# Optimization experiments

Hardware: AMD Instinct MI355X
Metric: run time of the kernel (lower is better)

## Reference

```python
import jax, jax.numpy as jnp
import numpy as np

H = 16          # num_attention_heads
DH = 64         # attention_head_size = hidden // heads
WINDOW = 128    # window_size
GLOBAL_RATIO = 0.1
SCALE = 1.0 / np.sqrt(DH)


def _combined_mask(seq_len):
    # sliding window: |i-j| <= window_size // 2
    pos = jnp.arange(seq_len)
    dist = pos[None, :] - pos[:, None]
    window_mask = jnp.abs(dist) <= (WINDOW // 2)
    # global tokens: first max(1, int(S * ratio)) positions, full row+col
    num_global = max(1, int(seq_len * GLOBAL_RATIO))
    is_global = pos < num_global
    global_mask = is_global[:, None] | is_global[None, :]
    return window_mask | global_mask  # [S, S] bool


def setup_inputs() -> dict:
    key = jax.random.key(0)
    ks = jax.random.split(key, 9)
    B, S, Dm = 2, 2048, 1024
    s = 0.02
    return {
        "hidden_states": jax.random.normal(ks[0], (B, S, Dm), jnp.float32),
        "Wq": jax.random.normal(ks[1], (Dm, Dm), jnp.float32) * s,
        "bq": jax.random.normal(ks[2], (Dm,), jnp.float32) * s,
        "Wk": jax.random.normal(ks[3], (Dm, Dm), jnp.float32) * s,
        "bk": jax.random.normal(ks[4], (Dm,), jnp.float32) * s,
        "Wv": jax.random.normal(ks[5], (Dm, Dm), jnp.float32) * s,
        "bv": jax.random.normal(ks[6], (Dm,), jnp.float32) * s,
        "Wo": jax.random.normal(ks[7], (Dm, Dm), jnp.float32) * s,
        "bo": jax.random.normal(ks[8], (Dm,), jnp.float32) * s,
    }


def reference(hidden_states, Wq, bq, Wk, bk, Wv, bv, Wo, bo):
    B, S, Dm = hidden_states.shape

    def heads(x):  # [B,S,Dm] -> [B,H,S,Dh]
        return x.reshape(B, S, H, DH).transpose(0, 2, 1, 3)

    q = heads(hidden_states @ Wq.T + bq)
    k = heads(hidden_states @ Wk.T + bk)
    v = heads(hidden_states @ Wv.T + bv)

    scores = jnp.einsum("bhqd,bhkd->bhqk", q, k) * SCALE
    mask = _combined_mask(S)  # [S,S] bool, True = attend
    scores = scores + jnp.where(mask, 0.0, -10000.0)[None, None]

    probs = jax.nn.softmax(scores, axis=-1)
    ctx = jnp.einsum("bhqk,bhkd->bhqd", probs, v)
    ctx = ctx.transpose(0, 2, 1, 3).reshape(B, S, Dm)
    return ctx @ Wo.T + bo
```

## Files before the change

### kernel.cpp

```cpp
#include <hip/hip_runtime.h>


#define B_   2
#define S_   2048
#define DM   1024
#define H_   16
#define NG   204
#define BS_  4096
#define SCL2 0.1803368801111204f
#define NEGF -3.0e38f

typedef unsigned short u16;
typedef unsigned int   u32;
typedef __attribute__((ext_vector_type(8))) short frag8;
typedef __attribute__((ext_vector_type(4))) short frag4;
typedef __attribute__((ext_vector_type(4))) float f32x4;

#define MFMA16(A, Bf, C) __builtin_amdgcn_mfma_f32_16x16x32_bf16((A), (Bf), (C), 0, 0, 0)

__device__ __forceinline__ f32x4 mfma_16x16x16_bf16(frag4 a, frag4 b, f32x4 c) {
#if defined(__HIP_DEVICE_COMPILE__)
  return __builtin_amdgcn_mfma_f32_16x16x16bf16_1k(a, b, c, 0, 0, 0);
#else
  (void)a; (void)b;
  return c;
#endif
}

#define GLD16(g, l)                                                              \
  __builtin_amdgcn_global_load_lds((const __attribute__((address_space(1))) u32*)(g), \
                                   (__attribute__((address_space(3))) u32*)(l), 16, 0, 0)
#define EXP2(x) exp2f(x)

__device__ __forceinline__ u16 f2bf(float f) {
  union { float f; u32 u; } c; c.f = f;
  u32 u = c.u + 0x7fffu + ((c.u >> 16) & 1u);
  return (u16)(u >> 16);
}

#if defined(__HIP_DEVICE_COMPILE__)
__device__ __forceinline__ u32 cvtpk_bf16(float lo, float hi) {
  u32 r;
  asm("v_cvt_pk_bf16_f32 %0, %1, %2" : "=v"(r) : "v"(lo), "v"(hi));
  return r;
}
#else
__device__ __forceinline__ u32 cvtpk_bf16(float lo, float hi) { (void)lo; (void)hi; return 0; }
#endif

__device__ __forceinline__ frag4 pack4_bf16(float a, float b, float c, float d) {
  union { u32 u[2]; frag4 f; } x;
  x.u[0] = cvtpk_bf16(a, b);
  x.u[1] = cvtpk_bf16(c, d);
  return x.f;
}

__global__ void cvt_all(const float* __restrict__ X,  const float* __restrict__ Wq,
                        const float* __restrict__ Wk, const float* __restrict__ Wv,
                        const float* __restrict__ Wo,
                        u16* Xb, u16* Wqb, u16* Wkb, u16* Wvb, u16* Wob) {
  const int chunk = blockIdx.y;
  const float* src; u16* dst;
  if (chunk < 4)      { src = X + (size_t)chunk * 1048576; dst = Xb + (size_t)chunk * 1048576; }
  else if (chunk == 4){ src = Wq; dst = Wqb; }
  else if (chunk == 5){ src = Wk; dst = Wkb; }
  else if (chunk == 6){ src = Wv; dst = Wvb; }
  else                { src = Wo; dst = Wob; }
  int i = blockIdx.x * 256 + threadIdx.x;
  float4 v = ((const float4*)src)[i];
  u32 lo = (u32)f2bf(v.x) | ((u32)f2bf(v.y) << 16);
  u32 hi = (u32)f2bf(v.z) | ((u32)f2bf(v.w) << 16);
  ((uint2*)dst)[i] = make_uint2(lo, hi);
}

__device__ __forceinline__ void gemm_mainloop(const u16* __restrict__ A, const u16* __restrict__ Bm,
                                              int bm, int bn, u16* As, u16* Bs,
                                              f32x4 acc[4][4]) {
  const int tid = threadIdx.x;
  const int wv = tid >> 6, lane = tid & 63, l15 = lane & 15, quad = lane >> 4;
  const int wm = wv & 1, wn = wv >> 1;

  const u16* gA[4]; const u16* gB[4];
#pragma unroll
  for (int c = 0; c < 4; ++c) {
    int idx = (wv * 4 + c) * 64 + lane;
    int r = idx >> 3;
    int cb = (idx & 7) ^ (r & 7);
    gA[c] = A  + (size_t)(bm + r) * DM + cb * 8;
    gB[c] = Bm + (size_t)(bn + r) * DM + cb * 8;
  }

  int offA[4][2], offB[4][2];
#pragma unroll
  for (int i = 0; i < 4; ++i)
#pragma unroll
    for (int h = 0; h < 2; ++h) {
      int mA = wm * 64 + i * 16 + l15;
      int mB = wn * 64 + i * 16 + l15;
      int cb = (quad + h * 4) ^ (l15 & 7);
      offA[i][h] = ((mA << 3) + cb) << 4;
      offB[i][h] = ((mB << 3) + cb) << 4;
    }

  for (int k0 = 0; k0 < DM; k0 += 64) {
#pragma unroll
    for (int c = 0; c < 4; ++c) {
      GLD16(gA[c] + k0, (char*)As + (wv * 4 + c) * 1024);
      GLD16(gB[c] + k0, (char*)Bs + (wv * 4 + c) * 1024);
    }
    __syncthreads();
    frag8 af[4][2], bf[4][2];
#pragma unroll
    for (int i = 0; i < 4; ++i) {
      af[i][0] = *(const frag8*)((const char*)As + offA[i][0]);
      af[i][1] = *(const frag8*)((const char*)As + offA[i][1]);
      bf[i][0] = *(const frag8*)((const char*)Bs + offB[i][0]);
      bf[i][1] = *(const frag8*)((const char*)Bs + offB[i][1]);
    }
#pragma unroll
    for (int h = 0; h < 2; ++h)
#pragma unroll
      for (int i = 0; i < 4; ++i)
#pragma unroll
        for (int j = 0; j < 4; ++j)
          acc[i][j] = MFMA16(af[i][h], bf[j][h], acc[i][j]);
    __syncthreads();
  }
}

__global__ __launch_bounds__(256, 3) void gemm_qkv(const u16* __restrict__ Xb,
    const u16* __restrict__ Wqb, const u16* __restrict__ Wkb, const u16* __restrict__ Wvb,
    const float* __restrict__ bq, const float* __restrict__ bk, const float* __restrict__ bv,
    u16* __restrict__ Qb, u16* __restrict__ Kb, u16* __restrict__ Vt) {
  __shared__ u16 As[8192], Bs[8192];
  const int bm = blockIdx.y * 128;
  const int which = blockIdx.x >> 3;
  const int bnl = (blockIdx.x & 7) * 128;
  const u16* W = (which == 0) ? Wqb : (which == 1) ? Wkb : Wvb;
  const float* bias = (which == 0) ? bq : (which == 1) ? bk : bv;

  f32x4 acc[4][4] = {};
  gemm_mainloop(Xb, W, bm, bnl, As, Bs, acc);

  const int tid = threadIdx.x, wv = tid >> 6, lane = tid & 63, l15 = lane & 15, quad = lane >> 4;
  const int wm = wv & 1, wn = wv >> 1;
  if (which < 2) {
    u16* O = (which == 0) ? Qb : Kb;
    const float scl = (which == 0) ? SCL2 : 1.0f;
#pragma unroll
    for (int j = 0; j < 4; ++j) {
      int col = bnl + wn * 64 + j * 16 + l15;
      float bb = bias[col];
#pragma unroll
      for (int i = 0; i < 4; ++i) {
        int row0 = bm + wm * 64 + i * 16 + quad * 4;
#pragma unroll
        for (int r = 0; r < 4; ++r)
          O[(size_t)(row0 + r) * DM + col] = f2bf((acc[i][j][r] + bb) * scl);
      }
    }
  } else {
#pragma unroll
    for (int j = 0; j < 4; ++j) {
      int col = bnl + wn * 64 + j * 16 + l15;
      float bb = bias[col];
#pragma unroll
      for (int i = 0; i < 4; ++i) {
        int row0 = bm + wm * 64 + i * 16 + quad * 4;
        u32 lo = (u32)f2bf(acc[i][j][0] + bb) | ((u32)f2bf(acc[i][j][1] + bb) << 16);
        u32 hi = (u32)f2bf(acc[i][j][2] + bb) | ((u32)f2bf(acc[i][j][3] + bb) << 16);
        *(uint2*)&Vt[(size_t)col * BS_ + row0] = make_uint2(lo, hi);
      }
    }
  }
}

__global__ __launch_bounds__(256, 3) void gemm_wo(const u16* __restrict__ Cx,
    const u16* __restrict__ Wob, const float* __restrict__ bo, float* __restrict__ out) {
  __shared__ u16 As[4096], Bs[8192];
  const int tid = threadIdx.x;
  const int wv = tid >> 6, lane = tid & 63, l15 = lane & 15, quad = lane >> 4;
  const int bm = blockIdx.y * 64, bn = blockIdx.x * 128;

  const u16* gA[2]; const u16* gB[4];
  int ldsA[2], ldsB[4];
#pragma unroll
  for (int c = 0; c < 2; ++c) {
    int slot = c * 256 + wv * 64 + lane;
    int r = slot >> 3, cb = (slot & 7) ^ (r & 7);
    gA[c] = Cx + (size_t)(bm + r) * DM + cb * 8;
    ldsA[c] = (c * 256 + wv * 64) * 16;
  }
#pragma unroll
  for (int c = 0; c < 4; ++c) {
    int slot = c * 256 + wv * 64 + lane;
    int r = slot >> 3, cb = (slot & 7) ^ (r & 7);
    gB[c] = Wob + (size_t)(bn + r) * DM + cb * 8;
    ldsB[c] = (c * 256 + wv * 64) * 16;
  }

  int offA[2], offB[8][2];
#pragma unroll
  for (int h = 0; h < 2; ++h) {
    int rowA = wv * 16 + l15;
    offA[h] = ((rowA << 3) + ((quad + h * 4) ^ (l15 & 7))) << 4;
#pragma unroll
    for (int j = 0; j < 8; ++j) {
      int rowB = j * 16 + l15;
      offB[j][h] = ((rowB << 3) + ((quad + h * 4) ^ (l15 & 7))) << 4;
    }
  }

  f32x4 acc[8] = {};
  for (int k0 = 0; k0 < DM; k0 += 64) {
#pragma unroll
    for (int c = 0; c < 2; ++c) GLD16(gA[c] + k0, (char*)As + ldsA[c]);
#pragma unroll
    for (int c = 0; c < 4; ++c) GLD16(gB[c] + k0, (char*)Bs + ldsB[c]);
    __syncthreads();
    frag8 af0 = *(const frag8*)((const char*)As + offA[0]);
    frag8 af1 = *(const frag8*)((const char*)As + offA[1]);
#pragma unroll
    for (int j = 0; j < 8; ++j) {
      frag8 bf0 = *(const frag8*)((const char*)Bs + offB[j][0]);
      frag8 bf1 = *(const frag8*)((const char*)Bs + offB[j][1]);
      acc[j] = MFMA16(af0, bf0, acc[j]);
      acc[j] = MFMA16(af1, bf1, acc[j]);
    }
    __syncthreads();
  }

#pragma unroll
  for (int j = 0; j < 8; ++j) {
    int col = bn + j * 16 + l15;
    float bb = bo[col];
    int row0 = bm + wv * 16 + quad * 4;
#pragma unroll
    for (int r = 0; r < 4; ++r)
      out[(size_t)(row0 + r) * DM + col] = acc[j][r] + bb;
  }
}

__global__ __launch_bounds__(256, 3) void attn_kernel(const u16* __restrict__ Q,
                                                      const u16* __restrict__ K,
                                                      const u16* __restrict__ Vt,
                                                      u16* __restrict__ Ctx,
                                                      float* __restrict__ Op,
                                                      float* __restrict__ Lp) {
  __shared__ u16 Ks[2][4096];
  __shared__ u16 Vs[2][4096];

  const int tid = threadIdx.x, w = tid >> 6, lane = tid & 63, l15 = lane & 15, quad = lane >> 4;
  const int blk = blockIdx.x;
  const int bh = blk & 31, unit = blk >> 5;
  const int b = bh >> 4, h = bh & 15;
  const bool heavy = unit < 8;
  const int strip = heavy ? (unit >> 2) : 0;
  const int q0 = heavy ? strip * 128 : 256 + (unit - 8) * 128;
  const int qw = q0 + w * 16;

  frag8 bq[2][2];
#pragma unroll
  for (int g = 0; g < 2; ++g) {
    const u16* qrow = Q + (size_t)(b * S_ + qw + g * 64 + l15) * DM + h * 64;
    bq[g][0] = *(const frag8*)(qrow + quad * 8);
    bq[g][1] = *(const frag8*)(qrow + quad * 8 + 32);
  }

  const u16* gK[2]; const u16* gV[2]; int ldso[2];
#pragma unroll
  for (int c = 0; c < 2; ++c) {
    int sl = (w * 2 + c) * 64 + lane;
    int r = sl >> 3;
    int fr = (r & 7) ^ (((r >> 3) & 1) << 2);
    int cb = (sl & 7) ^ fr;
    gK[c] = K  + (size_t)(b * S_ + r) * DM + h * 64 + cb * 8;
    gV[c] = Vt + (size_t)(h * 64 + r) * BS_ + (size_t)b * S_ + cb * 8;
    ldso[c] = (w * 2 + c) * 1024;
  }

  const int fl = (l15 & 7) ^ (((l15 >> 3) & 1) << 2);
  int offKb[2];
#pragma unroll
  for (int hh = 0; hh < 2; ++hh)
    offKb[hh] = ((l15 << 3) + ((quad + hh * 4) ^ fl)) << 4;
  int offVb[4];
#pragma unroll
  for (int kg = 0; kg < 4; ++kg)
    offVb[kg] = ((((l15 << 3) + ((((kg << 1) | (quad >> 1))) ^ fl)) << 4)
                 | ((quad & 1) << 3));

  int mlo[2]; u32 mspan[2];
#pragma unroll
  for (int g = 0; g < 2; ++g) {
    int qi = qw + g * 64 + l15;
    bool qg = qi < NG;
    mlo[g]   = qg ? (int)0x80000000 : (qi - 64);
    mspan[g] = qg ? 0xFFFFFFFFu : 128u;
  }
  const frag4 ones = {(short)0x3F80, (short)0x3F80, (short)0x3F80, (short)0x3F80};

  f32x4 o[2][4] = {};
  f32x4 o_l[2] = {};

  auto stage = [&](int t, int buf) {
#pragma unroll
    for (int c = 0; c < 2; ++c) {
      GLD16(gK[c] + (size_t)t * 64 * DM, (char*)Ks[buf] + ldso[c]);
      GLD16(gV[c] + t * 64,              (char*)Vs[buf] + ldso[c]);
    }
  };

  auto step = [&](int kt, int p, int mmode) {
    int gok0 = 1, gok1 = 1;
    if (mmode == 1) {
      const int k0s = kt * 64;
      const int ql1 = qw + 64;
      gok0 = (qw  < NG) || ((k0s + 63 >= qw  - 64) && (k0s <= qw  + 79));
      gok1 = (ql1 < NG) || ((k0s + 63 >= ql1 - 64) && (k0s <= ql1 + 79));
      if (!(gok0 | gok1)) return;
    }
    const char* kb_ = (const char*)Ks[p];
    const char* vb_ = (const char*)Vs[p];
    frag8 ak[4][2];
#pragma unroll
    for (int kg = 0; kg < 4; ++kg) {
      ak[kg][0] = *(const frag8*)(kb_ + offKb[0] + kg * 2048);
      ak[kg][1] = *(const frag8*)(kb_ + offKb[1] + kg * 2048);
    }
    const int k0 = kt * 64;
    const int gok[2] = {gok0, gok1};
    frag4 pk[2][4];
#pragma unroll
    for (int g = 0; g < 2; ++g) {
      if (!gok[g]) continue;
      f32x4 st[4] = {};
#pragma unroll
      for (int kg = 0; kg < 4; ++kg) {
        st[kg] = MFMA16(ak[kg][0], bq[g][0], st[kg]);
        st[kg] = MFMA16(ak[kg][1], bq[g][1], st[kg]);
      }
      if (mmode) {
#pragma unroll
        for (int kg = 0; kg < 4; ++kg) {
          float pr[4];
#pragma unroll
          for (int r = 0; r < 4; ++r) {
            int kc = k0 + kg * 16 + quad * 4 + r;
            bool act = ((u32)(kc - mlo[g]) <= mspan[g]);
            if (mmode == 2) act = act || (kc < NG);
            float e = EXP2(st[kg][r]);
            pr[r] = act ? e : 0.0f;
          }
          pk[g][kg] = pack4_bf16(pr[0], pr[1], pr[2], pr[3]);
        }
      } else {
#pragma unroll
        for (int kg = 0; kg < 4; ++kg)
          pk[g][kg] = pack4_bf16(EXP2(st[kg][0]), EXP2(st[kg][1]),
                                 EXP2(st[kg][2]), EXP2(st[kg][3]));
      }
    }
    if (gok0 & gok1) {
#pragma unroll
      for (int kg = 0; kg < 4; ++kg) {
        o_l[0] = mfma_16x16x16_bf16(ones, pk[0][kg], o_l[0]);
        o_l[1] = mfma_16x16x16_bf16(ones, pk[1][kg], o_l[1]);
#pragma unroll
        for (int nt = 0; nt < 4; ++nt) {
          frag4 av = *(const frag4*)(vb_ + offVb[kg] + nt * 2048);
          o[0][nt] = mfma_16x16x16_bf16(av, pk[0][kg], o[0][nt]);
          o[1][nt] = mfma_16x16x16_bf16(av, pk[1][kg], o[1][nt]);
        }
      }
    } else if (gok0) {
#pragma unroll
      for (int kg = 0; kg < 4; ++kg) {
        o_l[0] = mfma_16x16x16_bf16(ones, pk[0][kg], o_l[0]);
#pragma unroll
        for (int nt = 0; nt < 4; ++nt) {
          frag4 av = *(const frag4*)(vb_ + offVb[kg] + nt * 2048);
          o[0][nt] = mfma_16x16x16_bf16(av, pk[0][kg], o[0][nt]);
        }
      }
    } else {
#pragma unroll
      for (int kg = 0; kg < 4; ++kg) {
        o_l[1] = mfma_16x16x16_bf16(ones, pk[1][kg], o_l[1]);
#pragma unroll
        for (int nt = 0; nt < 4; ++nt) {
          frag4 av = *(const frag4*)(vb_ + offVb[kg] + nt * 2048);
          o[1][nt] = mfma_16x16x16_bf16(av, pk[1][kg], o[1][nt]);
        }
      }
    }
  };

  if (heavy) {
    const int seg = unit & 3;
    const int kt0 = seg * 8;
    const bool dm = (strip == 1);
    int p = 0;
    stage(kt0, 0);
#pragma unroll 1
    for (int tt = 0; tt < 8; ++tt) {
      __syncthreads();
      if (tt < 7) stage(kt0 + tt + 1, p ^ 1);
      const int kt = kt0 + tt;
      const int mm = dm ? ((kt == 3) ? 2 : ((kt > 2) ? 1 : 0)) : 0;
      step(kt, p, mm);
      p ^= 1;
    }
    float* op = Op + ((size_t)((bh * 2 + strip) * 4 + seg)) * 8192;
    float* lp = Lp + ((size_t)((bh * 2 + strip) * 4 + seg)) * 128;
#pragma unroll
    for (int g = 0; g < 2; ++g) {
      int rl = g * 64 + w * 16 + l15;
      if (quad == 0) lp[rl] = o_l[g][0];
#pragma unroll
      for (int nt = 0; nt < 4; ++nt)
        *(float4*)&op[rl * 64 + nt * 16 + quad * 4] =
            make_float4(o[g][nt][0], o[g][nt][1], o[g][nt][2], o[g][nt][3]);
    }
    return;
  }

  auto activef = [&](int t) {
    int k0 = t * 64;
    return (k0 < NG) || (k0 + 63 >= q0 - 64 && k0 <= q0 + 127 + 64);
  };
  auto nextt = [&](int cur) { int n = cur + 1; while (n < 32 && !activef(n)) ++n; return n; };

  int kt = 0, p = 0;
  stage(0, 0);
  for (;;) {
    int ktn = nextt(kt);
    bool more = ktn < 32;
    __syncthreads();
    if (more) stage(ktn, p ^ 1);
    const int mm = (kt == 3) ? 2 : ((kt > 2) ? 1 : 0);
    step(kt, p, mm);
    if (!more) break;
    kt = ktn; p ^= 1;
  }

#pragma unroll
  for (int g = 0; g < 2; ++g) {
    float inv = 1.0f / o_l[g][0];
    u16* crow = Ctx + (size_t)((size_t)b * S_ + qw + g * 64 + l15) * DM + h * 64;
#pragma unroll
    for (int nt = 0; nt < 4; ++nt) {
      u32 lo = (u32)f2bf(o[g][nt][0] * inv) | ((u32)f2bf(o[g][nt][1] * inv) << 16);
      u32 hi = (u32)f2bf(o[g][nt][2] * inv) | ((u32)f2bf(o[g][nt][3] * inv) << 16);
      *(uint2*)&crow[nt * 16 + quad * 4] = make_uint2(lo, hi);
    }
  }
}

__global__ __launch_bounds__(256) void combine_kernel(const float* __restrict__ Op,
                                                      const float* __restrict__ Lp,
                                                      u16* __restrict__ Ctx) {
  const int blk = blockIdx.x;
  const int bh = blk & 31, s64 = blk >> 5;
  const int b = bh >> 4, h = bh & 15;
  const int t = threadIdx.x;
  const int row = t >> 2, colg = (t & 3) * 16;
  const int gq = s64 * 64 + row;
  const int strip = gq >> 7, rIn = gq & 127;

  const float* opb = Op + ((size_t)(bh * 2 + strip) * 4) * 8192;
  const float* lpb = Lp + ((size_t)(bh * 2 + strip) * 4) * 128;

  float l = lpb[rIn] + lpb[128 + rIn] + lpb[256 + rIn] + lpb[384 + rIn];
  float acc[16];
#pragma unroll
  for (int e = 0; e < 16; ++e) acc[e] = opb[rIn * 64 + colg + e];
#pragma unroll
  for (int seg = 1; seg < 4; ++seg)
#pragma unroll
    for (int e = 0; e < 16; ++e) acc[e] += opb[seg * 8192 + rIn * 64 + colg + e];

  float inv = 1.0f / l;
  u32 pk[8];
#pragma unroll
  for (int p = 0; p < 8; ++p)
    pk[p] = (u32)f2bf(acc[2 * p] * inv) | ((u32)f2bf(acc[2 * p + 1] * inv) << 16);
  u16* dst = Ctx + (size_t)((size_t)b * S_ + gq) * DM + h * 64 + colg;
  *(uint4*)dst       = make_uint4(pk[0], pk[1], pk[2], pk[3]);
  *(uint4*)(dst + 8) = make_uint4(pk[4], pk[5], pk[6], pk[7]);
}

extern "C" void kernel_launch(void* const* d_in, const int* in_sizes, int n_in,
                              void* d_out, int out_size, void* d_ws, size_t ws_size,
                              hipStream_t stream) {
  const float* X  = (const float*)d_in[0];
  const float* Wq = (const float*)d_in[1];
  const float* bq = (const float*)d_in[2];
  const float* Wk = (const float*)d_in[3];
  const float* bk = (const float*)d_in[4];
  const float* Wv = (const float*)d_in[5];
  const float* bv = (const float*)d_in[6];
  const float* Wo = (const float*)d_in[7];
  const float* bo = (const float*)d_in[8];
  float* out = (float*)d_out;

  u16* ws = (u16*)d_ws;
  const size_t NX = (size_t)BS_ * DM;
  const size_t NW = (size_t)DM * DM;
  u16* Xb  = ws;
  u16* Wqb = Xb + NX;
  u16* Wkb = Wqb + NW;
  u16* Wvb = Wkb + NW;
  u16* Wob = Wvb + NW;
  u16* Qb  = Wob + NW;
  u16* Kb  = Qb + NX;
  u16* Vt  = Kb + NX;
  u16* Cx  = Vt + NX;
  float* Op = (float*)(Cx + NX);
  float* Lp = Op + (size_t)32 * 2 * 4 * 8192;

  cvt_all<<<dim3(1024, 8), 256, 0, stream>>>(X, Wq, Wk, Wv, Wo, Xb, Wqb, Wkb, Wvb, Wob);
  gemm_qkv<<<dim3(24, 32), 256, 0, stream>>>(Xb, Wqb, Wkb, Wvb, bq, bk, bv, Qb, Kb, Vt);
  attn_kernel<<<22 * 32, 256, 0, stream>>>(Qb, Kb, Vt, Cx, Op, Lp);
  combine_kernel<<<128, 256, 0, stream>>>(Op, Lp, Cx);
  gemm_wo<<<dim3(8, 64), 256, 0, stream>>>(Cx, Wob, bo, out);
}
```

Baseline: 173.9 us.

## Rewrite QKV projection GEMM with 256x192 tiles and double-buffered interleaved pipeline

Replaces the 128x128 single-buffered QKV GEMM with a 512-thread, 256x192-tile kernel. It treats the contiguous Wq/Wk/Wv bf16 buffers as one fused 3072-row weight matrix. Global-to-LDS loads are double-buffered with prefetch two steps ahead and interleaved between MFMA phases, using explicit barriers, waitcnts and setprio. A swizzled workgroup ID is added for L2 locality. The aim is to hide load latency and raise arithmetic intensity, at the cost of more LDS and registers, and it relies on the weight buffers being adjacent.

```diff
diff --git a/kernel.cpp b/kernel.cpp
--- a/kernel.cpp
+++ b/kernel.cpp
@@ -53,6 +53,16 @@
   x.u[0] = cvtpk_bf16(a, b);
   x.u[1] = cvtpk_bf16(c, d);
   return x.f;
+}
+
+__device__ __forceinline__ void wait_lgkm0() {
+  asm volatile("s_waitcnt lgkmcnt(0)" ::: "memory");
+  __builtin_amdgcn_sched_barrier(0);
+}
+__device__ __forceinline__ void hbar() {
+  __builtin_amdgcn_sched_barrier(0);
+  __builtin_amdgcn_s_barrier();
+  __builtin_amdgcn_sched_barrier(0);
 }
 
 __global__ void cvt_all(const float* __restrict__ X,  const float* __restrict__ Wq,
@@ -73,103 +83,184 @@
   ((uint2*)dst)[i] = make_uint2(lo, hi);
 }
 
-__device__ __forceinline__ void gemm_mainloop(const u16* __restrict__ A, const u16* __restrict__ Bm,
-                                              int bm, int bn, u16* As, u16* Bs,
-                                              f32x4 acc[4][4]) {
-  const int tid = threadIdx.x;
-  const int wv = tid >> 6, lane = tid & 63, l15 = lane & 15, quad = lane >> 4;
-  const int wm = wv & 1, wn = wv >> 1;
-
-  const u16* gA[4]; const u16* gB[4];
-#pragma unroll
-  for (int c = 0; c < 4; ++c) {
-    int idx = (wv * 4 + c) * 64 + lane;
-    int r = idx >> 3;
-    int cb = (idx & 7) ^ (r & 7);
-    gA[c] = A  + (size_t)(bm + r) * DM + cb * 8;
-    gB[c] = Bm + (size_t)(bn + r) * DM + cb * 8;
-  }
-
-  int offA[4][2], offB[4][2];
-#pragma unroll
-  for (int i = 0; i < 4; ++i)
-#pragma unroll
-    for (int h = 0; h < 2; ++h) {
-      int mA = wm * 64 + i * 16 + l15;
-      int mB = wn * 64 + i * 16 + l15;
-      int cb = (quad + h * 4) ^ (l15 & 7);
-      offA[i][h] = ((mA << 3) + cb) << 4;
-      offB[i][h] = ((mB << 3) + cb) << 4;
-    }
-
-  for (int k0 = 0; k0 < DM; k0 += 64) {
-#pragma unroll
-    for (int c = 0; c < 4; ++c) {
-      GLD16(gA[c] + k0, (char*)As + (wv * 4 + c) * 1024);
-      GLD16(gB[c] + k0, (char*)Bs + (wv * 4 + c) * 1024);
-    }
-    __syncthreads();
-    frag8 af[4][2], bf[4][2];
-#pragma unroll
-    for (int i = 0; i < 4; ++i) {
-      af[i][0] = *(const frag8*)((const char*)As + offA[i][0]);
-      af[i][1] = *(const frag8*)((const char*)As + offA[i][1]);
-      bf[i][0] = *(const frag8*)((const char*)Bs + offB[i][0]);
-      bf[i][1] = *(const frag8*)((const char*)Bs + offB[i][1]);
-    }
-#pragma unroll
-    for (int h = 0; h < 2; ++h)
-#pragma unroll
-      for (int i = 0; i < 4; ++i)
-#pragma unroll
-        for (int j = 0; j < 4; ++j)
-          acc[i][j] = MFMA16(af[i][h], bf[j][h], acc[i][j]);
-    __syncthreads();
-  }
-}
-
-__global__ __launch_bounds__(256, 3) void gemm_qkv(const u16* __restrict__ Xb,
-    const u16* __restrict__ Wqb, const u16* __restrict__ Wkb, const u16* __restrict__ Wvb,
+#define GQ_NT 16
+__global__ __launch_bounds__(512, 2) void gemm_qkv8(const u16* __restrict__ Xb,
+    const u16* __restrict__ Wall,
     const float* __restrict__ bq, const float* __restrict__ bk, const float* __restrict__ bv,
     u16* __restrict__ Qb, u16* __restrict__ Kb, u16* __restrict__ Vt) {
-  __shared__ u16 As[8192], Bs[8192];
-  const int bm = blockIdx.y * 128;
-  const int which = blockIdx.x >> 3;
-  const int bnl = (blockIdx.x & 7) * 128;
-  const u16* W = (which == 0) ? Wqb : (which == 1) ? Wkb : Wvb;
-  const float* bias = (which == 0) ? bq : (which == 1) ? bk : bv;
-
-  f32x4 acc[4][4] = {};
-  gemm_mainloop(Xb, W, bm, bnl, As, Bs, acc);
-
-  const int tid = threadIdx.x, wv = tid >> 6, lane = tid & 63, l15 = lane & 15, quad = lane >> 4;
+  __shared__ u16 As[2][16384];
+  __shared__ u16 Bs[2][12288];
+
+  const int tid = threadIdx.x, lane = tid & 63;
+  const int wv = tid >> 6, l15 = lane & 15, quad = lane >> 4;
   const int wm = wv & 1, wn = wv >> 1;
-  if (which < 2) {
-    u16* O = (which == 0) ? Qb : Kb;
-    const float scl = (which == 0) ? SCL2 : 1.0f;
-#pragma unroll
-    for (int j = 0; j < 4; ++j) {
-      int col = bnl + wn * 64 + j * 16 + l15;
-      float bb = bias[col];
-#pragma unroll
-      for (int i = 0; i < 4; ++i) {
-        int row0 = bm + wm * 64 + i * 16 + quad * 4;
+
+  const int bid = blockIdx.x;
+  const int wgid = (bid & 7) * 32 + (bid >> 3);
+  const int bm = (wgid >> 4) * 256;
+  const int bn = (wgid & 15) * 192;
+
+  const u16* srcA[4]; int ldsA[4];
+#pragma unroll
+  for (int g = 0; g < 4; ++g) {
+    int r = ((g & 1) << 7) + ((g >> 1) << 6) + (tid >> 3);
+    int c8 = (tid & 7) ^ (r & 7);
+    srcA[g] = Xb + (size_t)(bm + r) * DM + c8 * 8;
+    ldsA[g] = r * 128 + (tid & 7) * 16;
+  }
+  const u16* srcB[3]; int ldsB[3];
+#pragma unroll
+  for (int j = 0; j < 3; ++j) {
+    int sr = tid >> 3;
+    int rb = (sr >> 4) * 48 + j * 16 + (sr & 15);
+    int c8 = (tid & 7) ^ (rb & 7);
+    srcB[j] = Wall + (size_t)(bn + rb) * DM + c8 * 8;
+    ldsB[j] = rb * 128 + (tid & 7) * 16;
+  }
+
+  int offA[8][2], offB[3][2];
+#pragma unroll
+  for (int i = 0; i < 8; ++i)
+#pragma unroll
+    for (int h = 0; h < 2; ++h) {
+      int mA = wm * 128 + i * 16 + l15;
+      offA[i][h] = mA * 128 + (((quad + h * 4) ^ (l15 & 7)) << 4);
+    }
+#pragma unroll
+  for (int j = 0; j < 3; ++j)
+#pragma unroll
+    for (int h = 0; h < 2; ++h) {
+      int mB = wn * 48 + j * 16 + l15;
+      offB[j][h] = mB * 128 + (((quad + h * 4) ^ (l15 & 7)) << 4);
+    }
+
+  f32x4 acc[8][3] = {};
+  frag8 aL[4][2], aH[4][2], b01[2][2], b2[2];
+
+#pragma unroll
+  for (int g = 0; g < 2; ++g) GLD16(srcA[g], (char*)As[0] + ldsA[g]);
+#pragma unroll
+  for (int j = 0; j < 3; ++j) GLD16(srcB[j], (char*)Bs[0] + ldsB[j]);
+#pragma unroll
+  for (int g = 2; g < 4; ++g) GLD16(srcA[g], (char*)As[0] + ldsA[g]);
+#pragma unroll
+  for (int g = 0; g < 2; ++g) GLD16(srcA[g] + 64, (char*)As[1] + ldsA[g]);
+#pragma unroll
+  for (int j = 0; j < 3; ++j) GLD16(srcB[j] + 64, (char*)Bs[1] + ldsB[j]);
+#pragma unroll
+  for (int g = 2; g < 4; ++g) GLD16(srcA[g] + 64, (char*)As[1] + ldsA[g]);
+  asm volatile("s_waitcnt vmcnt(7)" ::: "memory");
+  hbar();
+
+#pragma unroll 1
+  for (int t = 0; t < GQ_NT; ++t) {
+    const char* Ab = (const char*)As[t & 1];
+    const char* Bb = (const char*)Bs[t & 1];
+    const int tp = t + 2;
+    const bool pf = (tp < GQ_NT);
+    const int ko = tp * 64;
+
+#pragma unroll
+    for (int i = 0; i < 4; ++i) {
+      aL[i][0] = *(const frag8*)(Ab + offA[i][0]);
+      aL[i][1] = *(const frag8*)(Ab + offA[i][1]);
+    }
+#pragma unroll
+    for (int j = 0; j < 2; ++j) {
+      b01[j][0] = *(const frag8*)(Bb + offB[j][0]);
+      b01[j][1] = *(const frag8*)(Bb + offB[j][1]);
+    }
+    hbar();
+    wait_lgkm0();
+    __builtin_amdgcn_s_setprio(1);
+#pragma unroll
+    for (int h = 0; h < 2; ++h)
+#pragma unroll
+      for (int i = 0; i < 4; ++i)
+#pragma unroll
+        for (int j = 0; j < 2; ++j)
+          acc[i][j] = MFMA16(aL[i][h], b01[j][h], acc[i][j]);
+    __builtin_amdgcn_s_setprio(0);
+    hbar();
+
+    b2[0] = *(const frag8*)(Bb + offB[2][0]);
+    b2[1] = *(const frag8*)(Bb + offB[2][1]);
+    if (pf) {
+      GLD16(srcA[0] + ko, (char*)As[tp & 1] + ldsA[0]);
+      GLD16(srcA[1] + ko, (char*)As[tp & 1] + ldsA[1]);
+      GLD16(srcB[0] + ko, (char*)Bs[tp & 1] + ldsB[0]);
+      GLD16(srcB[1] + ko, (char*)Bs[tp & 1] + ldsB[1]);
+    }
+    hbar();
+    wait_lgkm0();
+    __builtin_amdgcn_s_setprio(1);
+#pragma unroll
+    for (int h = 0; h < 2; ++h)
+#pragma unroll
+      for (int i = 0; i < 4; ++i)
+        acc[i][2] = MFMA16(aL[i][h], b2[h], acc[i][2]);
+    __builtin_amdgcn_s_setprio(0);
+    hbar();
+
+#pragma unroll
+    for (int i = 0; i < 4; ++i) {
+      aH[i][0] = *(const frag8*)(Ab + offA[4 + i][0]);
+      aH[i][1] = *(const frag8*)(Ab + offA[4 + i][1]);
+    }
+    if (pf) GLD16(srcB[2] + ko, (char*)Bs[tp & 1] + ldsB[2]);
+    hbar();
+    wait_lgkm0();
+    __builtin_amdgcn_s_setprio(1);
+#pragma unroll
+    for (int h = 0; h < 2; ++h)
+#pragma unroll
+      for (int i = 0; i < 4; ++i)
+#pragma unroll
+        for (int j = 0; j < 2; ++j)
+          acc[4 + i][j] = MFMA16(aH[i][h], b01[j][h], acc[4 + i][j]);
+    __builtin_amdgcn_s_setprio(0);
+    hbar();
+
+    if (pf) {
+      GLD16(srcA[2] + ko, (char*)As[tp & 1] + ldsA[2]);
+      GLD16(srcA[3] + ko, (char*)As[tp & 1] + ldsA[3]);
+    }
+    hbar();
+    __builtin_amdgcn_s_setprio(1);
+#pragma unroll
+    for (int h = 0; h < 2; ++h)
+#pragma unroll
+      for (int i = 0; i < 4; ++i)
+        acc[4 + i][2] = MFMA16(aH[i][h], b2[h], acc[4 + i][2]);
+    __builtin_amdgcn_s_setprio(0);
+    if (t < GQ_NT - 2) asm volatile("s_waitcnt vmcnt(7)" ::: "memory");
+    else               asm volatile("s_waitcnt vmcnt(0)" ::: "memory");
+    hbar();
+  }
+
+#pragma unroll
+  for (int j = 0; j < 3; ++j) {
+    int col = bn + wn * 48 + j * 16 + l15;
+    int which = col >> 10, lc = col & 1023;
+    const float* bias = (which == 0) ? bq : (which == 1) ? bk : bv;
+    float bb = bias[lc];
+    if (which < 2) {
+      u16* O = (which == 0) ? Qb : Kb;
+      const float scl = (which == 0) ? SCL2 : 1.0f;
+#pragma unroll
+      for (int i = 0; i < 8; ++i) {
+        int row0 = bm + wm * 128 + i * 16 + quad * 4;
 #pragma unroll
         for (int r = 0; r < 4; ++r)
-          O[(size_t)(row0 + r) * DM + col] = f2bf((acc[i][j][r] + bb) * scl);
+          O[(size_t)(row0 + r) * DM + lc] = f2bf((acc[i][j][r] + bb) * scl);
       }
-    }
-  } else {
-#pragma unroll
-    for (int j = 0; j < 4; ++j) {
-      int col = bnl + wn * 64 + j * 16 + l15;
-      float bb = bias[col];
-#pragma unroll
-      for (int i = 0; i < 4; ++i) {
-        int row0 = bm + wm * 64 + i * 16 + quad * 4;
+    } else {
+#pragma unroll
+      for (int i = 0; i < 8; ++i) {
+        int row0 = bm + wm * 128 + i * 16 + quad * 4;
         u32 lo = (u32)f2bf(acc[i][j][0] + bb) | ((u32)f2bf(acc[i][j][1] + bb) << 16);
         u32 hi = (u32)f2bf(acc[i][j][2] + bb) | ((u32)f2bf(acc[i][j][3] + bb) << 16);
-        *(uint2*)&Vt[(size_t)col * BS_ + row0] = make_uint2(lo, hi);
+        *(uint2*)&Vt[(size_t)lc * BS_ + row0] = make_uint2(lo, hi);
       }
     }
   }
@@ -520,7 +611,7 @@
   float* Lp = Op + (size_t)32 * 2 * 4 * 8192;
 
   cvt_all<<<dim3(1024, 8), 256, 0, stream>>>(X, Wq, Wk, Wv, Wo, Xb, Wqb, Wkb, Wvb, Wob);
-  gemm_qkv<<<dim3(24, 32), 256, 0, stream>>>(Xb, Wqb, Wkb, Wvb, bq, bk, bv, Qb, Kb, Vt);
+  gemm_qkv8<<<256, 512, 0, stream>>>(Xb, Wqb, bq, bk, bv, Qb, Kb, Vt);
   attn_kernel<<<22 * 32, 256, 0, stream>>>(Qb, Kb, Vt, Cx, Op, Lp);
   combine_kernel<<<128, 256, 0, stream>>>(Op, Lp, Cx);
   gemm_wo<<<dim3(8, 64), 256, 0, stream>>>(Cx, Wob, bo, out);
```

New measurement: 176.8 us. About the same (+1.7%).
